# Performance work log

Hardware: AMD Instinct MI355X
Metric: run time of the kernel (lower is better)

## Reference

```python
import jax, jax.numpy as jnp
import numpy as np

NUM_HEADS = 16


def setup_inputs() -> dict:
    key = jax.random.key(0)
    k1, k2, k3 = jax.random.split(key, 3)
    B, S, E = 2, 2048, 1024
    hidden_states = jax.random.normal(k1, (B, S, E), dtype=jnp.float32)
    c_attn_w = jax.random.normal(k2, (E, 3 * E), dtype=jnp.float32) * 0.02
    c_attn_b = jnp.zeros((3 * E,), dtype=jnp.float32)
    c_proj_w = jax.random.normal(k3, (E, E), dtype=jnp.float32) * 0.02
    c_proj_b = jnp.zeros((E,), dtype=jnp.float32)
    return {
        "hidden_states": hidden_states,
        "c_attn_w": c_attn_w,
        "c_attn_b": c_attn_b,
        "c_proj_w": c_proj_w,
        "c_proj_b": c_proj_b,
    }


def reference(hidden_states, c_attn_w, c_attn_b, c_proj_w, c_proj_b):
    B, S, E = hidden_states.shape
    H = NUM_HEADS
    D = E // H
    # Conv1D: qkv projection -> [B, S, 3E]
    qkv = jnp.einsum("bse,ef->bsf", hidden_states, c_attn_w) + c_attn_b
    q, k, v = jnp.split(qkv, 3, axis=-1)
    # split heads -> [B, H, S, D]
    def heads(x):
        return x.reshape(B, S, H, D).transpose(0, 2, 1, 3)
    q, k, v = heads(q), heads(k), heads(v)
    # scaled QK^T -> [B, H, S, S]
    scale = jnp.asarray(D, dtype=q.dtype) ** 0.5
    attn_weights = jnp.einsum("bhqd,bhkd->bhqk", q, k) / scale
    # causal mask (bias buffer): True on/below diagonal
    causal = jnp.tril(jnp.ones((S, S), dtype=bool))
    mask_value = jnp.finfo(attn_weights.dtype).min
    attn_weights = jnp.where(causal[None, None, :, :], attn_weights, mask_value)
    attn_weights = jax.nn.softmax(attn_weights, axis=-1)
    # attn @ V -> merge heads -> [B, S, E]
    attn_out = jnp.einsum("bhqk,bhkd->bhqd", attn_weights, v)
    attn_out = attn_out.transpose(0, 2, 1, 3).reshape(B, S, E)
    # output projection (Conv1D)
    out = jnp.einsum("bse,ef->bsf", attn_out, c_proj_w) + c_proj_b
    return out
```

## Files before the change

kernel.cpp:

```cpp
#include <hip/hip_runtime.h>
#include <stdint.h>

typedef __attribute__((ext_vector_type(8))) __bf16 bf16x8;
typedef __attribute__((ext_vector_type(4))) __bf16 bf16x4;
typedef __attribute__((ext_vector_type(4))) float f32x4;

#define MFMA16(a, b, c) __builtin_amdgcn_mfma_f32_16x16x32_bf16(a, b, c, 0, 0, 0)

__device__ __forceinline__ void async_ld16(const __bf16* g, __bf16* lds_base) {
    __builtin_amdgcn_global_load_lds(
        (const __attribute__((address_space(1))) void*)g,
        (__attribute__((address_space(3))) void*)lds_base, 16, 0, 0);
}

__global__ __launch_bounds__(256) void k_cast_bf16(const float* __restrict__ in,
                                                   __bf16* __restrict__ out, int n) {
    int i = (blockIdx.x * 256 + threadIdx.x) * 4;
    if (i >= n) return;
    float4 v = *(const float4*)(in + i);
    bf16x4 o;
    o.x = (__bf16)v.x; o.y = (__bf16)v.y; o.z = (__bf16)v.z; o.w = (__bf16)v.w;
    *(bf16x4*)(out + i) = o;
}

__global__ __launch_bounds__(256) void k_transpose_cast(const float* __restrict__ in,
                                                        __bf16* __restrict__ out,
                                                        int R, int C) {
    __shared__ __bf16 tile[32][33];
    int c0 = blockIdx.x * 32, r0 = blockIdx.y * 32;
    int tx = threadIdx.x, ty = threadIdx.y;
#pragma unroll
    for (int i = 0; i < 4; i++)
        tile[ty + i * 8][tx] = (__bf16)in[(size_t)(r0 + ty + i * 8) * C + c0 + tx];
    __syncthreads();
#pragma unroll
    for (int i = 0; i < 4; i++)
        out[(size_t)(c0 + ty + i * 8) * R + r0 + tx] = tile[tx][ty + i * 8];
}

__global__ __launch_bounds__(256, 2) void k_gemm_qkv(
    const __bf16* __restrict__ A, const __bf16* __restrict__ Bt,
    const float* __restrict__ bias,
    __bf16* __restrict__ Qo, __bf16* __restrict__ Ko, __bf16* __restrict__ Vo) {
    __shared__ __bf16 As[128 * 32];
    __shared__ __bf16 Bs[128 * 32];
    const int Kd = 1024;
    int n0 = blockIdx.x * 128, m0 = blockIdx.y * 128;
    int tid = threadIdx.x;
    int wv = tid >> 6, lane = tid & 63;
    int wm = (wv >> 1) * 64, wn = (wv & 1) * 64;
    int quad = lane >> 4, l16 = lane & 15;
    int lrow = lane >> 2, lcol = (lane & 3) * 8;
    f32x4 acc[4][4] = {};
    for (int k0 = 0; k0 < Kd; k0 += 32) {
        __syncthreads();
#pragma unroll
        for (int r = 0; r < 2; r++) {
            int row = r * 64 + wv * 16;
            async_ld16(&A[(size_t)(m0 + row + lrow) * Kd + k0 + lcol], &As[row * 32]);
            async_ld16(&Bt[(size_t)(n0 + row + lrow) * Kd + k0 + lcol], &Bs[row * 32]);
        }
        __syncthreads();
        bf16x8 af[4], bfr[4];
#pragma unroll
        for (int i = 0; i < 4; i++)
            af[i] = *(const bf16x8*)(&As[(wm + i * 16 + l16) * 32 + quad * 8]);
#pragma unroll
        for (int j = 0; j < 4; j++)
            bfr[j] = *(const bf16x8*)(&Bs[(wn + j * 16 + l16) * 32 + quad * 8]);
#pragma unroll
        for (int i = 0; i < 4; i++)
#pragma unroll
            for (int j = 0; j < 4; j++)
                acc[i][j] = MFMA16(af[i], bfr[j], acc[i][j]);
    }
#pragma unroll
    for (int i = 0; i < 4; i++) {
#pragma unroll
        for (int j = 0; j < 4; j++) {
            int n = n0 + wn + j * 16 + l16;
            float bv = bias[n];
            int sec = n >> 10, nl = n & 1023;
            int h = nl >> 6, d = nl & 63;
            int mbase = m0 + wm + i * 16 + quad * 4;
            int bb = mbase >> 11, s = mbase & 2047;
            if (sec == 2) {
                bf16x4 v4;
#pragma unroll
                for (int r = 0; r < 4; r++) v4[r] = (__bf16)(acc[i][j][r] + bv);
                *(bf16x4*)(&Vo[((size_t)(bb * 16 + h) * 64 + d) * 2048 + s]) = v4;
            } else {
                __bf16* dst = sec == 0 ? Qo : Ko;
                float scl = (sec == 0) ? 0.1803368801f : 1.0f;
#pragma unroll
                for (int r = 0; r < 4; r++)
                    dst[((size_t)(bb * 16 + h) * 2048 + (s + r)) * 64 + d] =
                        (__bf16)((acc[i][j][r] + bv) * scl);
            }
        }
    }
}

__global__ __launch_bounds__(256, 2) void k_gemm_proj(
    const __bf16* __restrict__ A, const __bf16* __restrict__ Bt,
    const float* __restrict__ bias, float* __restrict__ out) {
    __shared__ __bf16 As[64 * 32];
    __shared__ __bf16 Bs[128 * 32];
    const int Kd = 1024;
    int n0 = blockIdx.x * 128, m0 = blockIdx.y * 64;
    int tid = threadIdx.x;
    int wv = tid >> 6, lane = tid & 63;
    int wm = (wv >> 1) * 32, wn = (wv & 1) * 64;
    int quad = lane >> 4, l16 = lane & 15;
    int lrow = lane >> 2, lcol = (lane & 3) * 8;
    f32x4 acc[2][4] = {};
    for (int k0 = 0; k0 < Kd; k0 += 32) {
        __syncthreads();
        async_ld16(&A[(size_t)(m0 + wv * 16 + lrow) * Kd + k0 + lcol], &As[(wv * 16) * 32]);
#pragma unroll
        for (int r = 0; r < 2; r++) {
            int row = r * 64 + wv * 16;
            async_ld16(&Bt[(size_t)(n0 + row + lrow) * Kd + k0 + lcol], &Bs[row * 32]);
        }
        __syncthreads();
        bf16x8 af[2], bfr[4];
#pragma unroll
        for (int i = 0; i < 2; i++)
            af[i] = *(const bf16x8*)(&As[(wm + i * 16 + l16) * 32 + quad * 8]);
#pragma unroll
        for (int j = 0; j < 4; j++)
            bfr[j] = *(const bf16x8*)(&Bs[(wn + j * 16 + l16) * 32 + quad * 8]);
#pragma unroll
        for (int i = 0; i < 2; i++)
#pragma unroll
            for (int j = 0; j < 4; j++)
                acc[i][j] = MFMA16(af[i], bfr[j], acc[i][j]);
    }
#pragma unroll
    for (int i = 0; i < 2; i++) {
#pragma unroll
        for (int j = 0; j < 4; j++) {
            int n = n0 + wn + j * 16 + l16;
            float bv = bias[n];
#pragma unroll
            for (int r = 0; r < 4; r++) {
                int m = m0 + wm + i * 16 + quad * 4 + r;
                out[(size_t)m * 1024 + n] = acc[i][j][r] + bv;
            }
        }
    }
}

__device__ const int ATT_ORDER[24] = {7, 8, 10, 12, 14, 16, 18, 20, 22, 23, 6, 21,
                                      5, 19, 4, 17, 3, 15, 2, 13, 1, 11, 0, 9};

__global__ __launch_bounds__(256, 4) void k_attn(
    const __bf16* __restrict__ Qg, const __bf16* __restrict__ Kg,
    const __bf16* __restrict__ Vtg, __bf16* __restrict__ Op, float* __restrict__ Lp) {
    __shared__ __bf16 Ks[64 * 72];
    __shared__ __bf16 Vt[64 * 72];
    __shared__ __bf16 Ps[128 * 72];
    int bh = blockIdx.x & 31;
    int slot = ATT_ORDER[blockIdx.x >> 5];
    int t, k0, k1;
    if (slot < 8) { t = slot; k0 = 0; k1 = 2 * t + 2; }
    else { int i2 = slot - 8; t = 8 + (i2 >> 1); k0 = (i2 & 1) * 16; k1 = min(k0 + 16, 2 * t + 2); }
    const __bf16* Qp = Qg + (size_t)bh * 2048 * 64;
    const __bf16* Kp = Kg + (size_t)bh * 2048 * 64;
    const __bf16* Vp = Vtg + (size_t)bh * 64 * 2048;
    int tid = threadIdx.x, wv = tid >> 6, lane = tid & 63;
    int quad = lane >> 4, l16 = lane & 15;

    bf16x8 qf[2][2];
#pragma unroll
    for (int qn = 0; qn < 2; qn++)
#pragma unroll
        for (int ks = 0; ks < 2; ks++)
            qf[qn][ks] = *(const bf16x8*)(
                &Qp[(size_t)(t * 128 + wv * 32 + qn * 16 + l16) * 64 + ks * 32 + quad * 8]);
    float l_th[2] = {0.f, 0.f};
    f32x4 acc_o[2][4] = {};

    for (int kt = k0; kt < k1; kt++) {
        __syncthreads();
#pragma unroll
        for (int it = 0; it < 2; it++) {
            int idx = tid * 2 + it;
            int row = idx >> 3, cc = (idx & 7) * 8;
            *(uint4*)(&Ks[row * 72 + cc]) =
                *(const uint4*)(&Kp[(size_t)(kt * 64 + row) * 64 + cc]);
            *(uint4*)(&Vt[row * 72 + cc]) =
                *(const uint4*)(&Vp[(size_t)row * 2048 + kt * 64 + cc]);
        }
        __syncthreads();
        f32x4 s[2][4] = {};
#pragma unroll
        for (int ks = 0; ks < 2; ks++) {
            bf16x8 kf[4];
#pragma unroll
            for (int i = 0; i < 4; i++)
                kf[i] = *(const bf16x8*)(&Ks[(i * 16 + l16) * 72 + ks * 32 + quad * 8]);
#pragma unroll
            for (int i = 0; i < 4; i++)
#pragma unroll
                for (int qn = 0; qn < 2; qn++)
                    s[qn][i] = MFMA16(kf[i], qf[qn][ks], s[qn][i]);
        }
#pragma unroll
        for (int qn = 0; qn < 2; qn++) {
            int qmin = t * 128 + wv * 32 + qn * 16;
            if (kt * 64 + 63 > qmin) {
#pragma unroll
                for (int i = 0; i < 4; i++)
#pragma unroll
                    for (int r = 0; r < 4; r++)
                        if (kt * 64 + i * 16 + quad * 4 + r > qmin + l16) s[qn][i][r] = -1e30f;
            }
        }
#pragma unroll
        for (int qn = 0; qn < 2; qn++)
#pragma unroll
            for (int i = 0; i < 4; i++) {
                bf16x4 pk;
#pragma unroll
                for (int r = 0; r < 4; r++) {
                    float p = exp2f(s[qn][i][r]);
                    l_th[qn] += p;
                    pk[r] = (__bf16)p;
                }
                *(bf16x4*)(&Ps[(wv * 32 + qn * 16 + l16) * 72 + i * 16 + quad * 4]) = pk;
            }
#pragma unroll
        for (int ks = 0; ks < 2; ks++) {
            bf16x8 pf[2];
#pragma unroll
            for (int qn = 0; qn < 2; qn++)
                pf[qn] = *(const bf16x8*)(
                    &Ps[(wv * 32 + qn * 16 + l16) * 72 + ks * 32 + quad * 8]);
            bf16x8 vf[4];
#pragma unroll
            for (int i = 0; i < 4; i++)
                vf[i] = *(const bf16x8*)(&Vt[(i * 16 + l16) * 72 + ks * 32 + quad * 8]);
#pragma unroll
            for (int i = 0; i < 4; i++)
#pragma unroll
                for (int qn = 0; qn < 2; qn++)
                    acc_o[qn][i] = MFMA16(vf[i], pf[qn], acc_o[qn][i]);
        }
    }
    size_t pbase = (size_t)slot * 32 + bh;
#pragma unroll
    for (int qn = 0; qn < 2; qn++) {
        float ls = l_th[qn];
        ls += __shfl_xor(ls, 16);
        ls += __shfl_xor(ls, 32);
        int ql = wv * 32 + qn * 16 + l16;
        if (quad == 0) Lp[pbase * 128 + ql] = ls;
#pragma unroll
        for (int i = 0; i < 4; i++) {
            bf16x4 o4;
#pragma unroll
            for (int r = 0; r < 4; r++) o4[r] = (__bf16)acc_o[qn][i][r];
            *(bf16x4*)(&Op[(pbase * 128 + ql) * 64 + i * 16 + quad * 4]) = o4;
        }
    }
}

__global__ __launch_bounds__(256) void k_attn_combine(
    const __bf16* __restrict__ Op, const float* __restrict__ Lp,
    __bf16* __restrict__ AOb) {
    int gid = blockIdx.x * 256 + threadIdx.x;
    int d4 = gid & 15;
    int q = (gid >> 4) & 2047;
    int bh = gid >> 15;
    int t = q >> 7, ql = q & 127;
    int n = (t <= 7) ? 1 : 2;
    int base = (t <= 7) ? t : 8 + 2 * (t - 8);
    float L = 0.f, o[4] = {};
    for (int c = 0; c < n; c++) {
        size_t idx = (size_t)(base + c) * 32 + bh;
        L += Lp[idx * 128 + ql];
        bf16x4 p4 = *(const bf16x4*)(&Op[(idx * 128 + ql) * 64 + d4 * 4]);
#pragma unroll
        for (int r = 0; r < 4; r++) o[r] += (float)p4[r];
    }
    float inv = 1.f / L;
    int b = bh >> 4, h = bh & 15;
    bf16x4 o4;
#pragma unroll
    for (int r = 0; r < 4; r++) o4[r] = (__bf16)(o[r] * inv);
    *(bf16x4*)(&AOb[((size_t)b * 2048 + q) * 1024 + h * 64 + d4 * 4]) = o4;
}

extern "C" void kernel_launch(void* const* d_in, const int* in_sizes, int n_in,
                              void* d_out, int out_size, void* d_ws, size_t ws_size,
                              hipStream_t stream) {
    const float* hs = (const float*)d_in[0];
    const float* w1 = (const float*)d_in[1];
    const float* b1 = (const float*)d_in[2];
    const float* w2 = (const float*)d_in[3];
    const float* b2 = (const float*)d_in[4];
    float* out = (float*)d_out;

    char* ws = (char*)d_ws;
    __bf16* hsb = (__bf16*)(ws);
    __bf16* w1t = (__bf16*)(ws + (size_t)8 * 1024 * 1024);
    __bf16* w2t = (__bf16*)(ws + (size_t)14 * 1024 * 1024);
    __bf16* Qb  = (__bf16*)(ws + (size_t)16 * 1024 * 1024);
    __bf16* Kb  = (__bf16*)(ws + (size_t)24 * 1024 * 1024);
    __bf16* Vb  = (__bf16*)(ws + (size_t)32 * 1024 * 1024);
    __bf16* AOb = (__bf16*)(ws + (size_t)40 * 1024 * 1024);
    __bf16* Opart = (__bf16*)(ws);
    float*  Lpart = (float*)(ws + (size_t)13 * 1024 * 1024);

    k_cast_bf16<<<4096, 256, 0, stream>>>(hs, hsb, 4096 * 1024);
    k_transpose_cast<<<dim3(96, 32), dim3(32, 8), 0, stream>>>(w1, w1t, 1024, 3072);
    k_transpose_cast<<<dim3(32, 32), dim3(32, 8), 0, stream>>>(w2, w2t, 1024, 1024);
    k_gemm_qkv<<<dim3(24, 32), 256, 0, stream>>>(hsb, w1t, b1, Qb, Kb, Vb);
    k_attn<<<768, 256, 0, stream>>>(Qb, Kb, Vb, Opart, Lpart);
    k_attn_combine<<<4096, 256, 0, stream>>>(Opart, Lpart, AOb);
    k_gemm_proj<<<dim3(8, 64), 256, 0, stream>>>(AOb, w2t, b2, out);
}
```

Measured before the change: 187.4 us.

## Prefetch next K/V tile into registers in attention and merge prep kernels

Result: slower. 203.8 us (+8.7%).

```diff
diff --git a/kernel.cpp b/kernel.cpp
--- a/kernel.cpp
+++ b/kernel.cpp
@@ -13,22 +13,27 @@
         (__attribute__((address_space(3))) void*)lds_base, 16, 0, 0);
 }
 
-__global__ __launch_bounds__(256) void k_cast_bf16(const float* __restrict__ in,
-                                                   __bf16* __restrict__ out, int n) {
-    int i = (blockIdx.x * 256 + threadIdx.x) * 4;
-    if (i >= n) return;
-    float4 v = *(const float4*)(in + i);
-    bf16x4 o;
-    o.x = (__bf16)v.x; o.y = (__bf16)v.y; o.z = (__bf16)v.z; o.w = (__bf16)v.w;
-    *(bf16x4*)(out + i) = o;
-}
-
-__global__ __launch_bounds__(256) void k_transpose_cast(const float* __restrict__ in,
-                                                        __bf16* __restrict__ out,
-                                                        int R, int C) {
+__global__ __launch_bounds__(256) void k_prep(
+    const float* __restrict__ hs, const float* __restrict__ w1,
+    const float* __restrict__ w2, __bf16* __restrict__ hsb,
+    __bf16* __restrict__ w1t, __bf16* __restrict__ w2t) {
     __shared__ __bf16 tile[32][33];
-    int c0 = blockIdx.x * 32, r0 = blockIdx.y * 32;
-    int tx = threadIdx.x, ty = threadIdx.y;
+    int bid = blockIdx.x, tid = threadIdx.x;
+    if (bid < 4096) {
+        int i = (bid * 256 + tid) * 4;
+        float4 v = *(const float4*)(hs + i);
+        bf16x4 o;
+        o.x = (__bf16)v.x; o.y = (__bf16)v.y; o.z = (__bf16)v.z; o.w = (__bf16)v.w;
+        *(bf16x4*)(hsb + i) = o;
+        return;
+    }
+    const float* in; __bf16* out; int C, tb;
+    if (bid < 7168) { in = w1; out = w1t; C = 3072; tb = bid - 4096; }
+    else            { in = w2; out = w2t; C = 1024; tb = bid - 7168; }
+    const int R = 1024;
+    int ntc = C >> 5;
+    int c0 = (tb % ntc) * 32, r0 = (tb / ntc) * 32;
+    int tx = tid & 31, ty = tid >> 5;
 #pragma unroll
     for (int i = 0; i < 4; i++)
         tile[ty + i * 8][tx] = (__bf16)in[(size_t)(r0 + ty + i * 8) * C + c0 + tx];
@@ -170,6 +175,7 @@
     const __bf16* Vp = Vtg + (size_t)bh * 64 * 2048;
     int tid = threadIdx.x, wv = tid >> 6, lane = tid & 63;
     int quad = lane >> 4, l16 = lane & 15;
+    int srow = (tid * 2) >> 3, scc = ((tid * 2) & 7) * 8;
 
     bf16x8 qf[2][2];
 #pragma unroll
@@ -181,18 +187,25 @@
     float l_th[2] = {0.f, 0.f};
     f32x4 acc_o[2][4] = {};
 
+    {
+        const uint4* kg = (const uint4*)(&Kp[(size_t)(k0 * 64 + srow) * 64 + scc]);
+        const uint4* vg = (const uint4*)(&Vp[(size_t)srow * 2048 + k0 * 64 + scc]);
+        uint4 a = kg[0], bq = kg[1], x = vg[0], y = vg[1];
+        *(uint4*)(&Ks[srow * 72 + scc]) = a;
+        *(uint4*)(&Ks[srow * 72 + scc + 8]) = bq;
+        *(uint4*)(&Vt[srow * 72 + scc]) = x;
+        *(uint4*)(&Vt[srow * 72 + scc + 8]) = y;
+    }
+    __syncthreads();
+
     for (int kt = k0; kt < k1; kt++) {
-        __syncthreads();
-#pragma unroll
-        for (int it = 0; it < 2; it++) {
-            int idx = tid * 2 + it;
-            int row = idx >> 3, cc = (idx & 7) * 8;
-            *(uint4*)(&Ks[row * 72 + cc]) =
-                *(const uint4*)(&Kp[(size_t)(kt * 64 + row) * 64 + cc]);
-            *(uint4*)(&Vt[row * 72 + cc]) =
-                *(const uint4*)(&Vp[(size_t)row * 2048 + kt * 64 + cc]);
-        }
-        __syncthreads();
+        bool more = (kt + 1 < k1);
+        uint4 pk0, pk1, pv0, pv1;
+        if (more) {
+            const uint4* kg = (const uint4*)(&Kp[(size_t)((kt + 1) * 64 + srow) * 64 + scc]);
+            const uint4* vg = (const uint4*)(&Vp[(size_t)srow * 2048 + (kt + 1) * 64 + scc]);
+            pk0 = kg[0]; pk1 = kg[1]; pv0 = vg[0]; pv1 = vg[1];
+        }
         f32x4 s[2][4] = {};
 #pragma unroll
         for (int ks = 0; ks < 2; ks++) {
@@ -246,6 +259,14 @@
 #pragma unroll
                 for (int qn = 0; qn < 2; qn++)
                     acc_o[qn][i] = MFMA16(vf[i], pf[qn], acc_o[qn][i]);
+        }
+        if (more) {
+            __syncthreads();
+            *(uint4*)(&Ks[srow * 72 + scc]) = pk0;
+            *(uint4*)(&Ks[srow * 72 + scc + 8]) = pk1;
+            *(uint4*)(&Vt[srow * 72 + scc]) = pv0;
+            *(uint4*)(&Vt[srow * 72 + scc + 8]) = pv1;
+            __syncthreads();
         }
     }
     size_t pbase = (size_t)slot * 32 + bh;
@@ -313,9 +334,7 @@
     __bf16* Opart = (__bf16*)(ws);
     float*  Lpart = (float*)(ws + (size_t)13 * 1024 * 1024);
 
-    k_cast_bf16<<<4096, 256, 0, stream>>>(hs, hsb, 4096 * 1024);
-    k_transpose_cast<<<dim3(96, 32), dim3(32, 8), 0, stream>>>(w1, w1t, 1024, 3072);
-    k_transpose_cast<<<dim3(32, 32), dim3(32, 8), 0, stream>>>(w2, w2t, 1024, 1024);
+    k_prep<<<8192, 256, 0, stream>>>(hs, w1, w2, hsb, w1t, w2t);
     k_gemm_qkv<<<dim3(24, 32), 256, 0, stream>>>(hsb, w1t, b1, Qb, Kb, Vb);
     k_attn<<<768, 256, 0, stream>>>(Qb, Kb, Vb, Opart, Lpart);
     k_attn_combine<<<4096, 256, 0, stream>>>(Opart, Lpart, AOb);
```
